# Kernel tuning notes

Measured on AMD Instinct MI355X. Metric: run time of the kernel, lower is better.

Reference implementation:

```python
import jax, jax.numpy as jnp
import numpy as np

RC = 5.0
N_ATYPE = 10
ACSF_NMU = 20
APSF_NMU = 10
ACSF_ETA = 100.0
APSF_ETA = 25.0
N_ATOMS = 30000
N_PAIRS = 200000
MAX_NB = 6
DENSE = 64
FEAT_DIM = ACSF_NMU * N_ATYPE + APSF_NMU * N_ATYPE + 22  # 322
ZINDEX = jnp.array([1.0, 3.0, 5.0, 6.0, 7.0, 8.0, 9.0, 11.0, 15.0, 16.0])
CHARGE_KEYS = jnp.array([0.0, 1.0, 3.0, 5.0, 6.0, 7.0, 8.0, 9.0, 11.0, 15.0, 16.0])
CHARGE_VALS = jnp.array([100000, 0, 1, 2, 3, 4, 5, 6, 7, 8, 9])


def pbc_shift(dr, box, box_inv):
    ds = dr @ box_inv
    ds = ds - jnp.floor(ds + 0.5)
    return ds @ box


def int_to_onehot(labels, num_classes):
    zidx = CHARGE_VALS[jnp.searchsorted(CHARGE_KEYS, labels)]
    return jax.nn.one_hot(zidx, num_classes, dtype=labels.dtype)


def dense_ln_relu(x, W, b, g, beta):
    h = x @ W + b
    mu = jnp.mean(h, axis=-1, keepdims=True)
    var = jnp.mean(jnp.square(h - mu), axis=-1, keepdims=True)
    return jax.nn.relu((h - mu) * jax.lax.rsqrt(var + 1e-6) * g + beta)


def forward(pos, box, valid_mask, W1, b1, g1, be1, W2, b2, g2, be2, W3, b3, g3, be3, Wo, bo,
            pairs, topo_nblist, topo_mask, mol_ID, atype_indices):
    dt = pos.dtype
    acsf_mus = jnp.linspace(0.0, 5.0, ACSF_NMU).astype(dt)
    apsf_mus = jnp.linspace(-1.0, 1.0, APSF_NMU).astype(dt)
    mScales = jnp.array([0.0, 0.0, 0.0, 0.0, 0.0, 1.0], dtype=dt)
    # regularize_pairs: padded pairs have i >= j, shift them off-diagonal
    p = pairs[:, :2]
    dp_flag = (p[:, 1] - p[:, 0] <= 0).astype(p.dtype)
    p = p - jnp.stack([dp_flag, 2 * dp_flag], axis=1)
    nbonds = pairs[:, 2]
    buffer_scales = (p[:, 0] < p[:, 1]).astype(dt) * valid_mask
    mscales = mScales[nbonds - 1] * buffer_scales  # computed as in original (unused downstream)
    box_inv = jnp.linalg.inv(box)
    ri = pos[p[:, 0]]
    rj = pos[p[:, 1]]
    rij = pbc_shift(rj - ri, box, box_inv)
    dr_norm = jnp.linalg.norm(rij + 1e-10, axis=1)
    same_mol = mol_ID[p[:, 0]] == mol_ID[p[:, 1]]
    buffer_inter = jnp.where(same_mol, 0.0, 1.0).astype(dt)
    cutoff = jnp.where(dr_norm <= RC, 0.5 * (1 + jnp.cos(jnp.pi * dr_norm / RC)), 0.0)
    buffer_nblist_inter_rc = buffer_inter * buffer_scales * cutoff
    # environment atoms of each pair endpoint (bonded topology neighbors)
    j_nb = topo_nblist[p[:, 0]]  # [P, M]
    k_nb = topo_nblist[p[:, 1]]
    j_mask = topo_mask[p[:, 0]] & (j_nb != -1) & (j_nb != p[:, 0:1]) & (j_nb != p[:, 1:2])
    k_mask = topo_mask[p[:, 1]] & (k_nb != -1) & (k_nb != p[:, 0:1]) & (k_nb != p[:, 1:2])
    rij_unit = rij / (dr_norm[:, None] + 1e-10)

    def cos_gamma(center, nb, mask, unit):
        r_env = jnp.where(mask[..., None], pos[nb], 0.0)  # [P, M, 3]
        rX = pbc_shift(r_env - center[:, None, :], box, box_inv)
        rXn = rX / jnp.linalg.norm(rX + 1e-10, axis=2, keepdims=True)
        return jnp.einsum('pmi,pi->pm', rXn, unit) * mask

    cos_gamma_i = cos_gamma(ri, j_nb, j_mask, rij_unit)
    cos_gamma_j = cos_gamma(rj, k_nb, k_mask, -rij_unit)
    type_cols = jnp.arange(N_ATYPE)

    def apsf(cg, nb, mask):
        feat = jnp.exp(-APSF_ETA * jnp.square(cg[..., None] - apsf_mus)) * mask[..., None]
        onehot = (atype_indices[nb][..., None] == type_cols).astype(dt)
        return jnp.einsum('pmk,pml->pkl', feat, onehot)  # [P, APSF_NMU, N_ATYPE]

    G_pair = (apsf(cos_gamma_i, j_nb, j_mask) + apsf(cos_gamma_j, k_nb, k_mask)) * 0.5 \
             * buffer_nblist_inter_rc[:, None, None]
    # ACSF radial atom-centered features
    r_env = pos[topo_nblist]  # [N, M, 3]
    dr = pbc_shift(r_env - pos[:, None, :], box, box_inv)
    dnorm = jnp.linalg.norm(dr + 1e-10, axis=2)
    fx = dnorm / RC
    f_cut = jnp.where(fx < 1, 0.5 * (jnp.cos(jnp.pi * fx) + 1), 0.0) * topo_mask
    G_raw = jnp.exp(-ACSF_ETA * jnp.square(dnorm[..., None] - acsf_mus)) * f_cut[..., None]
    nb_onehot = (atype_indices[topo_nblist][..., None] == type_cols).astype(dt)
    G_atom = jnp.einsum('nmk,nml->nkl', G_raw, nb_onehot)  # [N, ACSF_NMU, N_ATYPE]
    atom_feat = 0.5 * (G_atom[p[:, 0]] + G_atom[p[:, 1]])
    # element charge + one-hot block
    elem = ZINDEX[atype_indices].astype(dt)
    j_z = elem[p[:, 0]]
    k_z = elem[p[:, 1]]
    atype_onehot = jnp.concatenate([j_z[:, None], int_to_onehot(j_z, 10),
                                    k_z[:, None], int_to_onehot(k_z, 10)], axis=1)
    feats = jnp.concatenate([atom_feat.reshape(atom_feat.shape[0], -1),
                             G_pair.reshape(G_pair.shape[0], -1),
                             atype_onehot], axis=1)  # [P, 322]
    # MLP energy head
    x = dense_ln_relu(feats, W1, b1, g1, be1)
    x = dense_ln_relu(x, W2, b2, g2, be2)
    x = dense_ln_relu(x, W3, b3, g3, be3)
    out_AB = x @ Wo + bo
    return jnp.sum(out_AB * buffer_nblist_inter_rc[:, None])


def setup_inputs() -> dict:
    key = jax.random.key(0)
    ks = jax.random.split(key, 16)
    L = 30.0
    pos = jax.random.uniform(ks[0], (N_ATOMS, 3), jnp.float32, 0.0, L)
    box = jnp.eye(3, dtype=jnp.float32) * L
    i = jax.random.randint(ks[1], (N_PAIRS,), 2, N_ATOMS)
    j = jax.random.randint(ks[2], (N_PAIRS,), 2, N_ATOMS)
    p0 = jnp.minimum(i, j)
    p1 = jnp.maximum(i, j)
    pairs = jnp.stack([p0, p1, jnp.full((N_PAIRS,), 6, dtype=p0.dtype)], axis=1)
    valid_mask = (jax.random.uniform(ks[3], (N_PAIRS,)) < 0.95).astype(jnp.float32)
    nb = jax.random.randint(ks[4], (N_ATOMS, MAX_NB), 0, N_ATOMS)
    topo_nblist = jnp.where(jax.random.uniform(ks[5], (N_ATOMS, MAX_NB)) < 0.25, -1, nb)
    topo_mask = topo_nblist != -1
    mol_ID = jnp.arange(N_ATOMS, dtype=jnp.int32) // 3
    atype_indices = jax.random.randint(ks[6], (N_ATOMS,), 0, N_ATYPE)

    def dense_w(k, fin, fout):
        return jax.random.normal(k, (fin, fout), jnp.float32) / np.float32(np.sqrt(fin))

    return {
        'pos': pos, 'box': box, 'valid_mask': valid_mask,
        'W1': dense_w(ks[7], FEAT_DIM, DENSE), 'b1': jnp.zeros((DENSE,), jnp.float32),
        'g1': jnp.ones((DENSE,), jnp.float32), 'be1': jnp.zeros((DENSE,), jnp.float32),
        'W2': dense_w(ks[8], DENSE, DENSE), 'b2': jnp.zeros((DENSE,), jnp.float32),
        'g2': jnp.ones((DENSE,), jnp.float32), 'be2': jnp.zeros((DENSE,), jnp.float32),
        'W3': dense_w(ks[9], DENSE, DENSE), 'b3': jnp.zeros((DENSE,), jnp.float32),
        'g3': jnp.ones((DENSE,), jnp.float32), 'be3': jnp.zeros((DENSE,), jnp.float32),
        'Wo': dense_w(ks[10], DENSE, 1), 'bo': jnp.zeros((1,), jnp.float32),
        'pairs': pairs, 'topo_nblist': topo_nblist, 'topo_mask': topo_mask,
        'mol_ID': mol_ID, 'atype_indices': atype_indices,
    }


def reference(pos, box, valid_mask, W1, b1, g1, be1, W2, b2, g2, be2, W3, b3, g3, be3, Wo, bo,
              pairs, topo_nblist, topo_mask, mol_ID, atype_indices):
    return forward(pos, box, valid_mask, W1, b1, g1, be1, W2, b2, g2, be2, W3, b3, g3, be3, Wo, bo,
                   pairs, topo_nblist, topo_mask, mol_ID, atype_indices)
```

## Files before the change

### kernel.cpp

```cpp
#include <hip/hip_runtime.h>
#include <math.h>

#define N_PAIRS_C 200000
#define MAX_NB_C 6
#define RC_F 5.0f
#define PI_F 3.14159265358979323846f
#define PPB 16
#define THREADS 256
#define NBLOCKS 256
#define FPAD 324
#define W1S 332
#define W23S 68

__device__ __constant__ float c_ZIND[10] = {1.f, 3.f, 5.f, 6.f, 7.f, 8.f, 9.f, 11.f, 15.f, 16.f};

__device__ __forceinline__ void invert3x3(const float* b, float* inv) {
    float a00 = b[0], a01 = b[1], a02 = b[2];
    float a10 = b[3], a11 = b[4], a12 = b[5];
    float a20 = b[6], a21 = b[7], a22 = b[8];
    float det = a00 * (a11 * a22 - a12 * a21)
              - a01 * (a10 * a22 - a12 * a20)
              + a02 * (a10 * a21 - a11 * a20);
    float id = 1.0f / det;
    inv[0] =  (a11 * a22 - a12 * a21) * id;
    inv[1] = -(a01 * a22 - a02 * a21) * id;
    inv[2] =  (a01 * a12 - a02 * a11) * id;
    inv[3] = -(a10 * a22 - a12 * a20) * id;
    inv[4] =  (a00 * a22 - a02 * a20) * id;
    inv[5] = -(a00 * a12 - a02 * a10) * id;
    inv[6] =  (a10 * a21 - a11 * a20) * id;
    inv[7] = -(a00 * a21 - a01 * a20) * id;
    inv[8] =  (a00 * a11 - a01 * a10) * id;
}

__device__ __forceinline__ void pbc3(float dx, float dy, float dz,
                                     const float* box, const float* binv,
                                     float& ox, float& oy, float& oz) {
    float s0 = dx * binv[0] + dy * binv[3] + dz * binv[6];
    float s1 = dx * binv[1] + dy * binv[4] + dz * binv[7];
    float s2 = dx * binv[2] + dy * binv[5] + dz * binv[8];
    s0 -= floorf(s0 + 0.5f);
    s1 -= floorf(s1 + 0.5f);
    s2 -= floorf(s2 + 0.5f);
    ox = s0 * box[0] + s1 * box[3] + s2 * box[6];
    oy = s0 * box[1] + s1 * box[4] + s2 * box[7];
    oz = s0 * box[2] + s1 * box[5] + s2 * box[8];
}

__device__ __forceinline__ float wsum64(float v) {
    #pragma unroll
    for (int off = 32; off > 0; off >>= 1) v += __shfl_xor(v, off, 64);
    return v;
}

__device__ __forceinline__ float ln_relu(float h, float g, float be) {
    float mu = wsum64(h) * 0.015625f;
    float d  = h - mu;
    float var = wsum64(d * d) * 0.015625f;
    float r = d * (1.0f / sqrtf(var + 1e-6f)) * g + be;
    return fmaxf(r, 0.0f);
}

__global__ void init_kernel(const float* __restrict__ box, float* __restrict__ binv,
                            int* __restrict__ counter) {
    if (threadIdx.x == 0) {
        invert3x3(box, binv);
        *counter = 0;
    }
}

__global__ __launch_bounds__(256) void filter_kernel(
        const float* __restrict__ pos,
        const float* __restrict__ box,
        const float* __restrict__ valid_mask,
        const int* __restrict__ pairs,
        const int* __restrict__ mol_ID,
        const float* __restrict__ binv,
        int* __restrict__ counter,
        int* __restrict__ act_p0,
        int* __restrict__ act_p1,
        float* __restrict__ act_fac,
        int max_active) {
    __shared__ int l_cnt, l_base;
    __shared__ int sp0[256], sp1[256];
    __shared__ float sfac[256];
    const int tid = threadIdx.x;
    if (tid == 0) l_cnt = 0;
    __syncthreads();

    int t = blockIdx.x * 256 + tid;
    bool keep = false;
    int p0 = 0, p1 = 0;
    float fac = 0.0f;
    if (t < N_PAIRS_C) {
        int i0 = pairs[3 * t], i1 = pairs[3 * t + 1];
        int dp = (i1 - i0 <= 0) ? 1 : 0;
        p0 = i0 - dp; p1 = i1 - 2 * dp;
        if (p0 < p1) {
            float vm = valid_mask[t];
            if (vm != 0.0f && mol_ID[p0] != mol_ID[p1]) {
                float dx, dy, dz;
                pbc3(pos[3 * p1] - pos[3 * p0],
                     pos[3 * p1 + 1] - pos[3 * p0 + 1],
                     pos[3 * p1 + 2] - pos[3 * p0 + 2], box, binv, dx, dy, dz);
                float ax = dx + 1e-10f, ay = dy + 1e-10f, az = dz + 1e-10f;
                float dn = sqrtf(ax * ax + ay * ay + az * az);
                if (dn <= RC_F) {
                    fac = vm * 0.5f * (1.0f + __cosf(PI_F * dn / RC_F));
                    keep = true;
                }
            }
        }
    }
    if (keep) {
        int slot = atomicAdd(&l_cnt, 1);
        sp0[slot] = p0; sp1[slot] = p1; sfac[slot] = fac;
    }
    __syncthreads();
    if (tid == 0) l_base = atomicAdd(counter, l_cnt);
    __syncthreads();
    if (tid < l_cnt) {
        int g = l_base + tid;
        if (g < max_active) {
            act_p0[g] = sp0[tid];
            act_p1[g] = sp1[tid];
            act_fac[g] = sfac[tid];
        }
    }
}

__global__ __launch_bounds__(THREADS) void mlp_kernel(
    const float* __restrict__ pos,
    const float* __restrict__ box,
    const float* __restrict__ W1, const float* __restrict__ b1,
    const float* __restrict__ g1, const float* __restrict__ be1,
    const float* __restrict__ W2, const float* __restrict__ b2,
    const float* __restrict__ g2, const float* __restrict__ be2,
    const float* __restrict__ W3, const float* __restrict__ b3,
    const float* __restrict__ g3, const float* __restrict__ be3,
    const float* __restrict__ Wo, const float* __restrict__ bo,
    const int* __restrict__ nblist,
    const int* __restrict__ atype,
    const float* __restrict__ binv,
    const int* __restrict__ counter,
    const int* __restrict__ act_p0,
    const int* __restrict__ act_p1,
    const float* __restrict__ act_fac,
    int max_active,
    float* __restrict__ partials) {

    __shared__ __align__(16) float W1t[64][W1S];
    __shared__ __align__(16) float W2t[64][W23S];
    __shared__ __align__(16) float W3t[64][W23S];
    __shared__ __align__(16) float feats[PPB][FPAD];
    __shared__ __align__(16) float xs[PPB][64];
    __shared__ float s_dn[PPB * 12], s_fc[PPB * 12], s_cg[PPB * 12];
    __shared__ int   s_ty[PPB * 12], s_av[PPB * 12], s_pv[PPB * 12];
    __shared__ int   s_p0[PPB], s_p1[PPB];
    __shared__ float s_fac[PPB], s_u[PPB][3], s_ri[PPB][3], s_rj[PPB][3];
    __shared__ float w_acc[4];

    const int tid = threadIdx.x;
    const int w = tid >> 6;
    const int j = tid & 63;

    int count = *counter;
    if (count > max_active) count = max_active;
    const int nq = (count + PPB - 1) / PPB;

    if (blockIdx.x >= nq) {
        if (tid == 0) partials[blockIdx.x] = 0.0f;
        return;
    }

    {
        const int fb0 = (tid >> 6) * 4;
        for (int base = 0; base < 324; base += 16) {
            int f = base + fb0;
            if (f < 324) {
                float4 v;
                v.x = (f + 0 < 322) ? W1[(f + 0) * 64 + j] : 0.0f;
                v.y = (f + 1 < 322) ? W1[(f + 1) * 64 + j] : 0.0f;
                v.z = (f + 2 < 322) ? W1[(f + 2) * 64 + j] : 0.0f;
                v.w = (f + 3 < 322) ? W1[(f + 3) * 64 + j] : 0.0f;
                *(float4*)&W1t[j][f] = v;
            }
        }
        for (int base = 0; base < 64; base += 16) {
            int f = base + fb0;
            float4 v2, v3;
            v2.x = W2[(f + 0) * 64 + j]; v3.x = W3[(f + 0) * 64 + j];
            v2.y = W2[(f + 1) * 64 + j]; v3.y = W3[(f + 1) * 64 + j];
            v2.z = W2[(f + 2) * 64 + j]; v3.z = W3[(f + 2) * 64 + j];
            v2.w = W2[(f + 3) * 64 + j]; v3.w = W3[(f + 3) * 64 + j];
            *(float4*)&W2t[j][f] = v2;
            *(float4*)&W3t[j][f] = v3;
        }
    }
    if (tid < 4) w_acc[tid] = 0.0f;

    float bx[9], bi[9];
    #pragma unroll
    for (int i = 0; i < 9; ++i) { bx[i] = box[i]; bi[i] = binv[i]; }

    const float b1j = b1[j], g1j = g1[j], be1j = be1[j];
    const float b2j = b2[j], g2j = g2[j], be2j = be2[j];
    const float b3j = b3[j], g3j = g3[j], be3j = be3[j];
    const float woj = Wo[j], bo0 = bo[0];

    const int q0 = 4 * w, q1 = 4 * w + 1, q2 = 4 * w + 2, q3 = 4 * w + 3;

    for (int q = blockIdx.x; q < nq; q += gridDim.x) {
        __syncthreads();

        for (int f = tid; f < PPB * FPAD; f += THREADS)
            ((float*)feats)[f] = 0.0f;
        if (tid < PPB) {
            int idx = q * PPB + tid;
            int p0 = 0, p1 = 0; float fac = 0.0f;
            if (idx < count) { p0 = act_p0[idx]; p1 = act_p1[idx]; fac = act_fac[idx]; }
            s_p0[tid] = p0; s_p1[tid] = p1; s_fac[tid] = fac;
            float rix = pos[3 * p0], riy = pos[3 * p0 + 1], riz = pos[3 * p0 + 2];
            float rjx = pos[3 * p1], rjy = pos[3 * p1 + 1], rjz = pos[3 * p1 + 2];
            s_ri[tid][0] = rix; s_ri[tid][1] = riy; s_ri[tid][2] = riz;
            s_rj[tid][0] = rjx; s_rj[tid][1] = rjy; s_rj[tid][2] = rjz;
            float dx, dy, dz;
            pbc3(rjx - rix, rjy - riy, rjz - riz, bx, bi, dx, dy, dz);
            float ax = dx + 1e-10f, ay = dy + 1e-10f, az = dz + 1e-10f;
            float dn0 = sqrtf(ax * ax + ay * ay + az * az);
            float idn = 1.0f / (dn0 + 1e-10f);
            s_u[tid][0] = dx * idn; s_u[tid][1] = dy * idn; s_u[tid][2] = dz * idn;
        }
        __syncthreads();

        if (tid < PPB * 12) {
            int pr = tid / 12, s = tid - pr * 12;
            float dn = 1.0f, fc = 0.0f, cg = 0.0f;
            int ty = 0, av = 0, pv = 0;
            int side = (s >= 6) ? 1 : 0;
            int m = side ? (s - 6) : s;
            int a = side ? s_p1[pr] : s_p0[pr];
            int nb = nblist[a * MAX_NB_C + m];
            if (nb != -1) {
                av = 1;
                float cx = side ? s_rj[pr][0] : s_ri[pr][0];
                float cy = side ? s_rj[pr][1] : s_ri[pr][1];
                float cz = side ? s_rj[pr][2] : s_ri[pr][2];
                float ex, ey, ez;
                pbc3(pos[3 * nb] - cx, pos[3 * nb + 1] - cy, pos[3 * nb + 2] - cz,
                     bx, bi, ex, ey, ez);
                float nx = ex + 1e-10f, ny = ey + 1e-10f, nz = ez + 1e-10f;
                dn = sqrtf(nx * nx + ny * ny + nz * nz);
                float fr = dn * (1.0f / RC_F);
                fc = (fr < 1.0f) ? 0.5f * (__cosf(PI_F * fr) + 1.0f) : 0.0f;
                ty = atype[nb];
                pv = (nb != s_p0[pr] && nb != s_p1[pr]) ? 1 : 0;
                float sgn = side ? -1.0f : 1.0f;
                cg = sgn * (ex * s_u[pr][0] + ey * s_u[pr][1] + ez * s_u[pr][2]) / dn;
            }
            s_dn[tid] = dn; s_fc[tid] = fc; s_cg[tid] = cg;
            s_ty[tid] = ty; s_av[tid] = av; s_pv[tid] = pv;
        } else if (tid < PPB * 12 + PPB) {
            int pr = tid - PPB * 12;
            int ti = atype[s_p0[pr]], tj = atype[s_p1[pr]];
            feats[pr][300] = c_ZIND[ti]; feats[pr][301 + ti] = 1.0f;
            feats[pr][311] = c_ZIND[tj]; feats[pr][312 + tj] = 1.0f;
        }
        __syncthreads();

        for (int task = tid; task < PPB * 360; task += THREADS) {
            if (task < PPB * 240) {
                int pr = task / 240, rem = task - pr * 240;
                int s = rem / 20, k = rem - s * 20;
                int base = pr * 12 + s;
                if (s_av[base] && s_fc[base] != 0.0f) {
                    float mu = (5.0f * (float)k) / 19.0f;
                    float d = s_dn[base] - mu;
                    atomicAdd(&feats[pr][k * 10 + s_ty[base]],
                              0.5f * __expf(-100.0f * d * d) * s_fc[base]);
                }
            } else {
                int u2 = task - PPB * 240;
                int pr = u2 / 120, rem = u2 - pr * 120;
                int s = rem / 10, k = rem - s * 10;
                int base = pr * 12 + s;
                if (s_pv[base]) {
                    float mu = -1.0f + (2.0f * (float)k) / 9.0f;
                    float d = s_cg[base] - mu;
                    atomicAdd(&feats[pr][200 + k * 10 + s_ty[base]],
                              0.5f * s_fac[pr] * __expf(-25.0f * d * d));
                }
            }
        }
        __syncthreads();

        const float4* w1row = (const float4*)&W1t[j][0];
        const float4* fA = (const float4*)&feats[q0][0];
        const float4* fB = (const float4*)&feats[q1][0];
        const float4* fC = (const float4*)&feats[q2][0];
        const float4* fD = (const float4*)&feats[q3][0];
        float hA = b1j, hB = b1j, hC = b1j, hD = b1j;
        #pragma unroll 3
        for (int g = 0; g < 81; ++g) {
            float4 wv = w1row[g];
            float4 a = fA[g], b = fB[g], c = fC[g], d = fD[g];
            hA = fmaf(a.x, wv.x, hA); hA = fmaf(a.y, wv.y, hA);
            hA = fmaf(a.z, wv.z, hA); hA = fmaf(a.w, wv.w, hA);
            hB = fmaf(b.x, wv.x, hB); hB = fmaf(b.y, wv.y, hB);
            hB = fmaf(b.z, wv.z, hB); hB = fmaf(b.w, wv.w, hB);
            hC = fmaf(c.x, wv.x, hC); hC = fmaf(c.y, wv.y, hC);
            hC = fmaf(c.z, wv.z, hC); hC = fmaf(c.w, wv.w, hC);
            hD = fmaf(d.x, wv.x, hD); hD = fmaf(d.y, wv.y, hD);
            hD = fmaf(d.z, wv.z, hD); hD = fmaf(d.w, wv.w, hD);
        }
        xs[q0][j] = ln_relu(hA, g1j, be1j);
        xs[q1][j] = ln_relu(hB, g1j, be1j);
        xs[q2][j] = ln_relu(hC, g1j, be1j);
        xs[q3][j] = ln_relu(hD, g1j, be1j);

        {
            const float4* xA = (const float4*)&xs[q0][0];
            const float4* xB = (const float4*)&xs[q1][0];
            const float4* xC = (const float4*)&xs[q2][0];
            const float4* xD = (const float4*)&xs[q3][0];
            float h2A = b2j, h2B = b2j, h2C = b2j, h2D = b2j;
            #pragma unroll
            for (int g = 0; g < 16; ++g) {
                float4 wv = *(const float4*)&W2t[j][4 * g];
                float4 a = xA[g], b = xB[g], c = xC[g], d = xD[g];
                h2A = fmaf(a.x, wv.x, h2A); h2A = fmaf(a.y, wv.y, h2A);
                h2A = fmaf(a.z, wv.z, h2A); h2A = fmaf(a.w, wv.w, h2A);
                h2B = fmaf(b.x, wv.x, h2B); h2B = fmaf(b.y, wv.y, h2B);
                h2B = fmaf(b.z, wv.z, h2B); h2B = fmaf(b.w, wv.w, h2B);
                h2C = fmaf(c.x, wv.x, h2C); h2C = fmaf(c.y, wv.y, h2C);
                h2C = fmaf(c.z, wv.z, h2C); h2C = fmaf(c.w, wv.w, h2C);
                h2D = fmaf(d.x, wv.x, h2D); h2D = fmaf(d.y, wv.y, h2D);
                h2D = fmaf(d.z, wv.z, h2D); h2D = fmaf(d.w, wv.w, h2D);
            }
            xs[q0][j] = ln_relu(h2A, g2j, be2j);
            xs[q1][j] = ln_relu(h2B, g2j, be2j);
            xs[q2][j] = ln_relu(h2C, g2j, be2j);
            xs[q3][j] = ln_relu(h2D, g2j, be2j);
        }
        {
            const float4* xA = (const float4*)&xs[q0][0];
            const float4* xB = (const float4*)&xs[q1][0];
            const float4* xC = (const float4*)&xs[q2][0];
            const float4* xD = (const float4*)&xs[q3][0];
            float h3A = b3j, h3B = b3j, h3C = b3j, h3D = b3j;
            #pragma unroll
            for (int g = 0; g < 16; ++g) {
                float4 wv = *(const float4*)&W3t[j][4 * g];
                float4 a = xA[g], b = xB[g], c = xC[g], d = xD[g];
                h3A = fmaf(a.x, wv.x, h3A); h3A = fmaf(a.y, wv.y, h3A);
                h3A = fmaf(a.z, wv.z, h3A); h3A = fmaf(a.w, wv.w, h3A);
                h3B = fmaf(b.x, wv.x, h3B); h3B = fmaf(b.y, wv.y, h3B);
                h3B = fmaf(b.z, wv.z, h3B); h3B = fmaf(b.w, wv.w, h3B);
                h3C = fmaf(c.x, wv.x, h3C); h3C = fmaf(c.y, wv.y, h3C);
                h3C = fmaf(c.z, wv.z, h3C); h3C = fmaf(c.w, wv.w, h3C);
                h3D = fmaf(d.x, wv.x, h3D); h3D = fmaf(d.y, wv.y, h3D);
                h3D = fmaf(d.z, wv.z, h3D); h3D = fmaf(d.w, wv.w, h3D);
            }
            float rA = wsum64(ln_relu(h3A, g3j, be3j) * woj);
            float rB = wsum64(ln_relu(h3B, g3j, be3j) * woj);
            float rC = wsum64(ln_relu(h3C, g3j, be3j) * woj);
            float rD = wsum64(ln_relu(h3D, g3j, be3j) * woj);
            if (j == 0) {
                w_acc[w] += (rA + bo0) * s_fac[q0] + (rB + bo0) * s_fac[q1]
                          + (rC + bo0) * s_fac[q2] + (rD + bo0) * s_fac[q3];
            }
        }
    }
    __syncthreads();
    if (tid == 0)
        partials[blockIdx.x] = w_acc[0] + w_acc[1] + w_acc[2] + w_acc[3];
}

__global__ void reduce_kernel(const float* __restrict__ partials, float* __restrict__ out) {
    __shared__ float ws[4];
    const int tid = threadIdx.x;
    float v = partials[tid];
    v = wsum64(v);
    if ((tid & 63) == 0) ws[tid >> 6] = v;
    __syncthreads();
    if (tid == 0) out[0] = ws[0] + ws[1] + ws[2] + ws[3];
}

extern "C" void kernel_launch(void* const* d_in, const int* in_sizes, int n_in,
                              void* d_out, int out_size, void* d_ws, size_t ws_size,
                              hipStream_t stream) {
    const float* pos        = (const float*)d_in[0];
    const float* box        = (const float*)d_in[1];
    const float* valid_mask = (const float*)d_in[2];
    const float* W1  = (const float*)d_in[3];
    const float* b1  = (const float*)d_in[4];
    const float* g1  = (const float*)d_in[5];
    const float* be1 = (const float*)d_in[6];
    const float* W2  = (const float*)d_in[7];
    const float* b2  = (const float*)d_in[8];
    const float* g2  = (const float*)d_in[9];
    const float* be2 = (const float*)d_in[10];
    const float* W3  = (const float*)d_in[11];
    const float* b3  = (const float*)d_in[12];
    const float* g3  = (const float*)d_in[13];
    const float* be3 = (const float*)d_in[14];
    const float* Wo  = (const float*)d_in[15];
    const float* bo  = (const float*)d_in[16];
    const int* pairs = (const int*)d_in[17];
    const int* nbl   = (const int*)d_in[18];
    const int* mol   = (const int*)d_in[20];
    const int* aty   = (const int*)d_in[21];

    char* ws = (char*)d_ws;
    int*   counter  = (int*)ws;
    float* binv     = (float*)(ws + 16);
    float* partials = (float*)(ws + 64);
    char*  actbase  = ws + 64 + NBLOCKS * 4;
    long long cap_ll = ((long long)ws_size - (64 + NBLOCKS * 4)) / 12;
    int cap = (cap_ll > 0) ? (int)cap_ll : 0;
    if (cap > N_PAIRS_C) cap = N_PAIRS_C;
    int*   act_p0  = (int*)actbase;
    int*   act_p1  = act_p0 + cap;
    float* act_fac = (float*)(act_p1 + cap);

    float* out = (float*)d_out;

    init_kernel<<<1, 64, 0, stream>>>(box, binv, counter);
    filter_kernel<<<(N_PAIRS_C + 255) / 256, 256, 0, stream>>>(
        pos, box, valid_mask, pairs, mol, binv, counter,
        act_p0, act_p1, act_fac, cap);
    mlp_kernel<<<NBLOCKS, THREADS, 0, stream>>>(
        pos, box,
        W1, b1, g1, be1, W2, b2, g2, be2, W3, b3, g3, be3, Wo, bo,
        nbl, aty, binv, counter, act_p0, act_p1, act_fac, cap, partials);
    reduce_kernel<<<1, NBLOCKS, 0, stream>>>(partials, out);
}
```

Measured before the change: 48.31 us.

## Fuse pair filtering, MLP and reduction into one kernel with per-block compaction

Merges the filter, MLP and reduce kernels into a single kernel. Each block filters a fixed slice of pairs into a shared-memory list and runs the MLP on those pairs directly. The final sum uses a float atomic accumulator and a ticket counter instead of a separate reduction launch. This removes two launches and the global compaction buffer round-trip. In exchange, load balancing now depends on how active pairs are spread across slices, and any slice with more than 192 active pairs would silently drop the extras.

```diff
diff --git a/kernel.cpp b/kernel.cpp
--- a/kernel.cpp
+++ b/kernel.cpp
@@ -7,7 +7,9 @@
 #define PI_F 3.14159265358979323846f
 #define PPB 16
 #define THREADS 256
-#define NBLOCKS 256
+#define NB 256
+#define SLICE 782
+#define LCAP 192
 #define FPAD 324
 #define W1S 332
 #define W23S 68
@@ -62,76 +64,18 @@
 }
 
 __global__ void init_kernel(const float* __restrict__ box, float* __restrict__ binv,
-                            int* __restrict__ counter) {
+                            int* __restrict__ ticket, float* __restrict__ accum) {
     if (threadIdx.x == 0) {
         invert3x3(box, binv);
-        *counter = 0;
-    }
-}
-
-__global__ __launch_bounds__(256) void filter_kernel(
-        const float* __restrict__ pos,
-        const float* __restrict__ box,
-        const float* __restrict__ valid_mask,
-        const int* __restrict__ pairs,
-        const int* __restrict__ mol_ID,
-        const float* __restrict__ binv,
-        int* __restrict__ counter,
-        int* __restrict__ act_p0,
-        int* __restrict__ act_p1,
-        float* __restrict__ act_fac,
-        int max_active) {
-    __shared__ int l_cnt, l_base;
-    __shared__ int sp0[256], sp1[256];
-    __shared__ float sfac[256];
-    const int tid = threadIdx.x;
-    if (tid == 0) l_cnt = 0;
-    __syncthreads();
-
-    int t = blockIdx.x * 256 + tid;
-    bool keep = false;
-    int p0 = 0, p1 = 0;
-    float fac = 0.0f;
-    if (t < N_PAIRS_C) {
-        int i0 = pairs[3 * t], i1 = pairs[3 * t + 1];
-        int dp = (i1 - i0 <= 0) ? 1 : 0;
-        p0 = i0 - dp; p1 = i1 - 2 * dp;
-        if (p0 < p1) {
-            float vm = valid_mask[t];
-            if (vm != 0.0f && mol_ID[p0] != mol_ID[p1]) {
-                float dx, dy, dz;
-                pbc3(pos[3 * p1] - pos[3 * p0],
-                     pos[3 * p1 + 1] - pos[3 * p0 + 1],
-                     pos[3 * p1 + 2] - pos[3 * p0 + 2], box, binv, dx, dy, dz);
-                float ax = dx + 1e-10f, ay = dy + 1e-10f, az = dz + 1e-10f;
-                float dn = sqrtf(ax * ax + ay * ay + az * az);
-                if (dn <= RC_F) {
-                    fac = vm * 0.5f * (1.0f + __cosf(PI_F * dn / RC_F));
-                    keep = true;
-                }
-            }
-        }
-    }
-    if (keep) {
-        int slot = atomicAdd(&l_cnt, 1);
-        sp0[slot] = p0; sp1[slot] = p1; sfac[slot] = fac;
-    }
-    __syncthreads();
-    if (tid == 0) l_base = atomicAdd(counter, l_cnt);
-    __syncthreads();
-    if (tid < l_cnt) {
-        int g = l_base + tid;
-        if (g < max_active) {
-            act_p0[g] = sp0[tid];
-            act_p1[g] = sp1[tid];
-            act_fac[g] = sfac[tid];
-        }
-    }
-}
-
-__global__ __launch_bounds__(THREADS) void mlp_kernel(
+        *ticket = 0;
+        *accum = 0.0f;
+    }
+}
+
+__global__ __launch_bounds__(THREADS) void fused_kernel(
     const float* __restrict__ pos,
     const float* __restrict__ box,
+    const float* __restrict__ valid_mask,
     const float* __restrict__ W1, const float* __restrict__ b1,
     const float* __restrict__ g1, const float* __restrict__ be1,
     const float* __restrict__ W2, const float* __restrict__ b2,
@@ -139,15 +83,14 @@
     const float* __restrict__ W3, const float* __restrict__ b3,
     const float* __restrict__ g3, const float* __restrict__ be3,
     const float* __restrict__ Wo, const float* __restrict__ bo,
+    const int* __restrict__ pairs,
     const int* __restrict__ nblist,
     const int* __restrict__ atype,
+    const int* __restrict__ mol_ID,
     const float* __restrict__ binv,
-    const int* __restrict__ counter,
-    const int* __restrict__ act_p0,
-    const int* __restrict__ act_p1,
-    const float* __restrict__ act_fac,
-    int max_active,
-    float* __restrict__ partials) {
+    int* __restrict__ ticket,
+    float* __restrict__ accum,
+    float* __restrict__ out) {
 
     __shared__ __align__(16) float W1t[64][W1S];
     __shared__ __align__(16) float W2t[64][W23S];
@@ -158,23 +101,25 @@
     __shared__ int   s_ty[PPB * 12], s_av[PPB * 12], s_pv[PPB * 12];
     __shared__ int   s_p0[PPB], s_p1[PPB];
     __shared__ float s_fac[PPB], s_u[PPB][3], s_ri[PPB][3], s_rj[PPB][3];
+    __shared__ int   l_p0[LCAP], l_p1[LCAP];
+    __shared__ float l_fac[LCAP];
+    __shared__ int   l_cnt;
     __shared__ float w_acc[4];
 
     const int tid = threadIdx.x;
     const int w = tid >> 6;
     const int j = tid & 63;
 
-    int count = *counter;
-    if (count > max_active) count = max_active;
-    const int nq = (count + PPB - 1) / PPB;
-
-    if (blockIdx.x >= nq) {
-        if (tid == 0) partials[blockIdx.x] = 0.0f;
-        return;
-    }
+    float bx[9], bi[9];
+    #pragma unroll
+    for (int i = 0; i < 9; ++i) { bx[i] = box[i]; bi[i] = binv[i]; }
+
+    if (tid == 0) l_cnt = 0;
+    if (tid < 4) w_acc[tid] = 0.0f;
+    __syncthreads();
 
     {
-        const int fb0 = (tid >> 6) * 4;
+        const int fb0 = w * 4;
         for (int base = 0; base < 324; base += 16) {
             int f = base + fb0;
             if (f < 324) {
@@ -197,11 +142,36 @@
             *(float4*)&W3t[j][f] = v3;
         }
     }
-    if (tid < 4) w_acc[tid] = 0.0f;
-
-    float bx[9], bi[9];
-    #pragma unroll
-    for (int i = 0; i < 9; ++i) { bx[i] = box[i]; bi[i] = binv[i]; }
+
+    {
+        int base = blockIdx.x * SLICE;
+        int lim = base + SLICE;
+        if (lim > N_PAIRS_C) lim = N_PAIRS_C;
+        for (int t = base + tid; t < lim; t += THREADS) {
+            int i0 = pairs[3 * t], i1 = pairs[3 * t + 1];
+            int dp = (i1 - i0 <= 0) ? 1 : 0;
+            int p0 = i0 - dp, p1 = i1 - 2 * dp;
+            if (p0 >= p1) continue;
+            float vm = valid_mask[t];
+            if (vm == 0.0f) continue;
+            if (mol_ID[p0] == mol_ID[p1]) continue;
+            float dx, dy, dz;
+            pbc3(pos[3 * p1] - pos[3 * p0],
+                 pos[3 * p1 + 1] - pos[3 * p0 + 1],
+                 pos[3 * p1 + 2] - pos[3 * p0 + 2], bx, bi, dx, dy, dz);
+            float ax = dx + 1e-10f, ay = dy + 1e-10f, az = dz + 1e-10f;
+            float dn = sqrtf(ax * ax + ay * ay + az * az);
+            if (dn > RC_F) continue;
+            float fac = vm * 0.5f * (1.0f + __cosf(PI_F * dn / RC_F));
+            int slot = atomicAdd(&l_cnt, 1);
+            if (slot < LCAP) { l_p0[slot] = p0; l_p1[slot] = p1; l_fac[slot] = fac; }
+        }
+    }
+    __syncthreads();
+
+    int cnt = l_cnt;
+    if (cnt > LCAP) cnt = LCAP;
+    const int nchunks = (cnt + PPB - 1) / PPB;
 
     const float b1j = b1[j], g1j = g1[j], be1j = be1[j];
     const float b2j = b2[j], g2j = g2[j], be2j = be2[j];
@@ -210,15 +180,15 @@
 
     const int q0 = 4 * w, q1 = 4 * w + 1, q2 = 4 * w + 2, q3 = 4 * w + 3;
 
-    for (int q = blockIdx.x; q < nq; q += gridDim.x) {
+    for (int c = 0; c < nchunks; ++c) {
         __syncthreads();
 
         for (int f = tid; f < PPB * FPAD; f += THREADS)
             ((float*)feats)[f] = 0.0f;
         if (tid < PPB) {
-            int idx = q * PPB + tid;
+            int idx = c * PPB + tid;
             int p0 = 0, p1 = 0; float fac = 0.0f;
-            if (idx < count) { p0 = act_p0[idx]; p1 = act_p1[idx]; fac = act_fac[idx]; }
+            if (idx < cnt) { p0 = l_p0[idx]; p1 = l_p1[idx]; fac = l_fac[idx]; }
             s_p0[tid] = p0; s_p1[tid] = p1; s_fac[tid] = fac;
             float rix = pos[3 * p0], riy = pos[3 * p0 + 1], riz = pos[3 * p0 + 2];
             float rjx = pos[3 * p1], rjy = pos[3 * p1 + 1], rjz = pos[3 * p1 + 2];
@@ -303,13 +273,13 @@
         #pragma unroll 3
         for (int g = 0; g < 81; ++g) {
             float4 wv = w1row[g];
-            float4 a = fA[g], b = fB[g], c = fC[g], d = fD[g];
+            float4 a = fA[g], b = fB[g], c2 = fC[g], d = fD[g];
             hA = fmaf(a.x, wv.x, hA); hA = fmaf(a.y, wv.y, hA);
             hA = fmaf(a.z, wv.z, hA); hA = fmaf(a.w, wv.w, hA);
             hB = fmaf(b.x, wv.x, hB); hB = fmaf(b.y, wv.y, hB);
             hB = fmaf(b.z, wv.z, hB); hB = fmaf(b.w, wv.w, hB);
-            hC = fmaf(c.x, wv.x, hC); hC = fmaf(c.y, wv.y, hC);
-            hC = fmaf(c.z, wv.z, hC); hC = fmaf(c.w, wv.w, hC);
+            hC = fmaf(c2.x, wv.x, hC); hC = fmaf(c2.y, wv.y, hC);
+            hC = fmaf(c2.z, wv.z, hC); hC = fmaf(c2.w, wv.w, hC);
             hD = fmaf(d.x, wv.x, hD); hD = fmaf(d.y, wv.y, hD);
             hD = fmaf(d.z, wv.z, hD); hD = fmaf(d.w, wv.w, hD);
         }
@@ -327,13 +297,13 @@
             #pragma unroll
             for (int g = 0; g < 16; ++g) {
                 float4 wv = *(const float4*)&W2t[j][4 * g];
-                float4 a = xA[g], b = xB[g], c = xC[g], d = xD[g];
+                float4 a = xA[g], b = xB[g], c2 = xC[g], d = xD[g];
                 h2A = fmaf(a.x, wv.x, h2A); h2A = fmaf(a.y, wv.y, h2A);
                 h2A = fmaf(a.z, wv.z, h2A); h2A = fmaf(a.w, wv.w, h2A);
                 h2B = fmaf(b.x, wv.x, h2B); h2B = fmaf(b.y, wv.y, h2B);
                 h2B = fmaf(b.z, wv.z, h2B); h2B = fmaf(b.w, wv.w, h2B);
-                h2C = fmaf(c.x, wv.x, h2C); h2C = fmaf(c.y, wv.y, h2C);
-                h2C = fmaf(c.z, wv.z, h2C); h2C = fmaf(c.w, wv.w, h2C);
+                h2C = fmaf(c2.x, wv.x, h2C); h2C = fmaf(c2.y, wv.y, h2C);
+                h2C = fmaf(c2.z, wv.z, h2C); h2C = fmaf(c2.w, wv.w, h2C);
                 h2D = fmaf(d.x, wv.x, h2D); h2D = fmaf(d.y, wv.y, h2D);
                 h2D = fmaf(d.z, wv.z, h2D); h2D = fmaf(d.w, wv.w, h2D);
             }
@@ -351,13 +321,13 @@
             #pragma unroll
             for (int g = 0; g < 16; ++g) {
                 float4 wv = *(const float4*)&W3t[j][4 * g];
-                float4 a = xA[g], b = xB[g], c = xC[g], d = xD[g];
+                float4 a = xA[g], b = xB[g], c2 = xC[g], d = xD[g];
                 h3A = fmaf(a.x, wv.x, h3A); h3A = fmaf(a.y, wv.y, h3A);
                 h3A = fmaf(a.z, wv.z, h3A); h3A = fmaf(a.w, wv.w, h3A);
                 h3B = fmaf(b.x, wv.x, h3B); h3B = fmaf(b.y, wv.y, h3B);
                 h3B = fmaf(b.z, wv.z, h3B); h3B = fmaf(b.w, wv.w, h3B);
-                h3C = fmaf(c.x, wv.x, h3C); h3C = fmaf(c.y, wv.y, h3C);
-                h3C = fmaf(c.z, wv.z, h3C); h3C = fmaf(c.w, wv.w, h3C);
+                h3C = fmaf(c2.x, wv.x, h3C); h3C = fmaf(c2.y, wv.y, h3C);
+                h3C = fmaf(c2.z, wv.z, h3C); h3C = fmaf(c2.w, wv.w, h3C);
                 h3D = fmaf(d.x, wv.x, h3D); h3D = fmaf(d.y, wv.y, h3D);
                 h3D = fmaf(d.z, wv.z, h3D); h3D = fmaf(d.w, wv.w, h3D);
             }
@@ -372,18 +342,18 @@
         }
     }
     __syncthreads();
-    if (tid == 0)
-        partials[blockIdx.x] = w_acc[0] + w_acc[1] + w_acc[2] + w_acc[3];
-}
-
-__global__ void reduce_kernel(const float* __restrict__ partials, float* __restrict__ out) {
-    __shared__ float ws[4];
-    const int tid = threadIdx.x;
-    float v = partials[tid];
-    v = wsum64(v);
-    if ((tid & 63) == 0) ws[tid >> 6] = v;
-    __syncthreads();
-    if (tid == 0) out[0] = ws[0] + ws[1] + ws[2] + ws[3];
+
+    if (tid == 0) {
+        float partial = w_acc[0] + w_acc[1] + w_acc[2] + w_acc[3];
+        atomicAdd(accum, partial);
+        __threadfence();
+        int old = atomicAdd(ticket, 1);
+        if (old == NB - 1) {
+            __threadfence();
+            float tot = atomicAdd(accum, 0.0f);
+            out[0] = tot;
+        }
+    }
 }
 
 extern "C" void kernel_launch(void* const* d_in, const int* in_sizes, int n_in,
@@ -412,26 +382,15 @@
     const int* aty   = (const int*)d_in[21];
 
     char* ws = (char*)d_ws;
-    int*   counter  = (int*)ws;
-    float* binv     = (float*)(ws + 16);
-    float* partials = (float*)(ws + 64);
-    char*  actbase  = ws + 64 + NBLOCKS * 4;
-    long long cap_ll = ((long long)ws_size - (64 + NBLOCKS * 4)) / 12;
-    int cap = (cap_ll > 0) ? (int)cap_ll : 0;
-    if (cap > N_PAIRS_C) cap = N_PAIRS_C;
-    int*   act_p0  = (int*)actbase;
-    int*   act_p1  = act_p0 + cap;
-    float* act_fac = (float*)(act_p1 + cap);
+    int*   ticket = (int*)ws;
+    float* accum  = (float*)(ws + 16);
+    float* binv   = (float*)(ws + 32);
 
     float* out = (float*)d_out;
 
-    init_kernel<<<1, 64, 0, stream>>>(box, binv, counter);
-    filter_kernel<<<(N_PAIRS_C + 255) / 256, 256, 0, stream>>>(
-        pos, box, valid_mask, pairs, mol, binv, counter,
-        act_p0, act_p1, act_fac, cap);
-    mlp_kernel<<<NBLOCKS, THREADS, 0, stream>>>(
-        pos, box,
+    init_kernel<<<1, 64, 0, stream>>>(box, binv, ticket, accum);
+    fused_kernel<<<NB, THREADS, 0, stream>>>(
+        pos, box, valid_mask,
         W1, b1, g1, be1, W2, b2, g2, be2, W3, b3, g3, be3, Wo, bo,
-        nbl, aty, binv, counter, act_p0, act_p1, act_fac, cap, partials);
-    reduce_kernel<<<1, NBLOCKS, 0, stream>>>(partials, out);
-}
+        pairs, nbl, aty, mol, binv, ticket, accum, out);
+}
```

Result: slower. 57.79 us (+19.6%).
